# Kernel tuning notes

Hardware: AMD Instinct MI355X
Metric: run time of the kernel (lower is better)

Reference implementation:

```python
import jax, jax.numpy as jnp
import numpy as np


def _dequantize(packed, scales, zero_points):
    # packed: [out, in//2] holding two INT4 values per byte (low nibble = even col,
    # high nibble = odd col). Returns fp32 weight [out, in].
    low = (packed & 0xF).astype(jnp.float32)
    high = ((packed >> 4) & 0xF).astype(jnp.float32)
    w = jnp.stack([low, high], axis=-1).reshape(packed.shape[0], -1)  # [out, in]
    return (w - zero_points[:, None]) * scales[:, None]


def setup_inputs() -> dict:
    key = jax.random.key(0)
    k_x, k_w, k_s, k_z = jax.random.split(key, 4)
    TOKENS, IN_F, OUT_F = 8192, 4096, 14336
    x = jax.random.normal(k_x, (TOKENS, IN_F), dtype=jnp.float32)
    packed_weights = jax.random.randint(k_w, (OUT_F, IN_F // 2), 0, 256, dtype=jnp.int32)
    scales = jax.random.uniform(k_s, (OUT_F,), dtype=jnp.float32) * 0.01 + 1e-4
    zero_points = jax.random.uniform(k_z, (OUT_F,), dtype=jnp.float32) * 15.0
    return {"x": x, "packed_weights": packed_weights, "scales": scales,
            "zero_points": zero_points}


def reference(x, packed_weights, scales, zero_points):
    w_fp32 = _dequantize(packed_weights, scales, zero_points)  # [out, in]
    return x @ w_fp32.T  # [tokens, out]
```

## Files before the change

kernel.cpp:

```cpp
#include <hip/hip_runtime.h>
#include <hip/hip_bf16.h>


typedef __bf16 bf16x8 __attribute__((ext_vector_type(8)));
typedef __bf16 bf16x4 __attribute__((ext_vector_type(4)));
typedef float floatx4 __attribute__((ext_vector_type(4)));

#define M_DIM 8192
#define K_DIM 4096
#define N_DIM 14336
#define KB    (K_DIM / 2)

#define BM 128
#define BN 128
#define BK 64
#define LDSK 72

__global__ __launch_bounds__(256) void qgemm_bf16(
    const float* __restrict__ X,
    const int*   __restrict__ P,
    const float* __restrict__ S,
    const float* __restrict__ Z,
    float*       __restrict__ O)
{
    __shared__ __bf16 Alds[BM * LDSK];
    __shared__ __bf16 Blds[BN * LDSK];

    const int t  = threadIdx.x;
    const int bn = blockIdx.x;
    const int bm = blockIdx.y;

    const int rowA0 = t >> 4;
    const int c4    = t & 15;
    const int rowB0 = t >> 3;
    const int cB    = t & 7;

    const float* aG = X + (size_t)(bm * BM + rowA0) * K_DIM + c4 * 4;
    const int*   bG = P + (size_t)(bn * BN + rowB0) * KB    + cB * 4;

    float sreg[4], oreg[4];
    for (int it = 0; it < 4; ++it) {
        int r = bn * BN + rowB0 + 32 * it;
        float s = S[r], z = Z[r];
        sreg[it] = s;
        oreg[it] = -z * s;
    }

    const int lane = t & 63;
    const int wave = t >> 6;
    const int wm   = wave >> 1;
    const int wn   = wave & 1;
    const int fr   = lane & 15;
    const int quad = lane >> 4;

    floatx4 acc[4][4];
    for (int i = 0; i < 4; ++i)
        for (int j = 0; j < 4; ++j)
            acc[i][j] = (floatx4)0.0f;

    const __bf16* aBase = &Alds[(wm * 64 + fr) * LDSK + quad * 8];
    const __bf16* bBase = &Blds[(wn * 64 + fr) * LDSK + quad * 8];

    for (int kt = 0; kt < K_DIM / BK; ++kt) {
        float4 av[8];
        for (int it = 0; it < 8; ++it)
            av[it] = *(const float4*)(aG + (size_t)it * 16 * K_DIM);
        int4 bv[4];
        for (int it = 0; it < 4; ++it)
            bv[it] = *(const int4*)(bG + (size_t)it * 32 * KB);
        aG += BK;
        bG += BK / 2;

        for (int it = 0; it < 8; ++it) {
            bf16x4 w;
            w[0] = (__bf16)av[it].x;
            w[1] = (__bf16)av[it].y;
            w[2] = (__bf16)av[it].z;
            w[3] = (__bf16)av[it].w;
            *(bf16x4*)&Alds[(rowA0 + 16 * it) * LDSK + c4 * 4] = w;
        }
        for (int it = 0; it < 4; ++it) {
            const float s = sreg[it], o = oreg[it];
            const int b0 = bv[it].x, b1 = bv[it].y, b2 = bv[it].z, b3 = bv[it].w;
            bf16x8 w;
            w[0] = (__bf16)((float)(b0 & 15) * s + o);
            w[1] = (__bf16)((float)((b0 >> 4) & 15) * s + o);
            w[2] = (__bf16)((float)(b1 & 15) * s + o);
            w[3] = (__bf16)((float)((b1 >> 4) & 15) * s + o);
            w[4] = (__bf16)((float)(b2 & 15) * s + o);
            w[5] = (__bf16)((float)((b2 >> 4) & 15) * s + o);
            w[6] = (__bf16)((float)(b3 & 15) * s + o);
            w[7] = (__bf16)((float)((b3 >> 4) & 15) * s + o);
            *(bf16x8*)&Blds[(rowB0 + 32 * it) * LDSK + cB * 8] = w;
        }
        __syncthreads();

        for (int kk = 0; kk < BK; kk += 32) {
            bf16x8 af[4], bf[4];
            for (int i = 0; i < 4; ++i)
                af[i] = *(const bf16x8*)(aBase + (i * 16) * LDSK + kk);
            for (int j = 0; j < 4; ++j)
                bf[j] = *(const bf16x8*)(bBase + (j * 16) * LDSK + kk);
            for (int i = 0; i < 4; ++i)
                for (int j = 0; j < 4; ++j)
                    acc[i][j] = __builtin_amdgcn_mfma_f32_16x16x32_bf16(
                        af[i], bf[j], acc[i][j], 0, 0, 0);
        }
        __syncthreads();
    }

    for (int i = 0; i < 4; ++i) {
        const int row = bm * BM + wm * 64 + i * 16 + quad * 4;
        for (int j = 0; j < 4; ++j) {
            const int col = bn * BN + wn * 64 + j * 16 + fr;
            float* o = O + (size_t)row * N_DIM + col;
            for (int r = 0; r < 4; ++r)
                o[(size_t)r * N_DIM] = acc[i][j][r];
        }
    }
}

extern "C" void kernel_launch(void* const* d_in, const int* in_sizes, int n_in,
                              void* d_out, int out_size, void* d_ws, size_t ws_size,
                              hipStream_t stream) {
    const float* x = (const float*)d_in[0];
    const int*   p = (const int*)d_in[1];
    const float* s = (const float*)d_in[2];
    const float* z = (const float*)d_in[3];
    float* out = (float*)d_out;

    dim3 grid(N_DIM / BN, M_DIM / BM);
    qgemm_bf16<<<grid, 256, 0, stream>>>(x, p, s, z, out);
}
```

Before: 1.827 ms.

## Pre-convert X and dequantize W to bf16, then run async-LDS GEMM

Splits the fused kernel into three passes: convert X to bf16 and dequantize the INT4 weights to bf16 into workspace buffers, then run a plain bf16 GEMM. The GEMM loads tiles straight into LDS with global_load_lds and remaps workgroups with a swizzle so neighbouring blocks share L2 data. This removes the per-tile conversion and dequant work that every block repeated, and the register staging of loads. In exchange it writes and rereads about 180 MB of workspace, uses unpadded LDS rows that may cause bank conflicts, and falls back to the old kernel if the workspace is too small.

```diff
diff --git a/kernel.cpp b/kernel.cpp
--- a/kernel.cpp
+++ b/kernel.cpp
@@ -15,6 +15,126 @@
 #define BN 128
 #define BK 64
 #define LDSK 72
+
+__device__ __forceinline__ void async_ld16(const __bf16* g, __bf16* l) {
+    __builtin_amdgcn_global_load_lds(
+        (const __attribute__((address_space(1))) void*)g,
+        (__attribute__((address_space(3))) void*)l,
+        16, 0, 0);
+}
+
+__global__ __launch_bounds__(256) void cvt_x_kernel(
+    const float* __restrict__ X, __bf16* __restrict__ XB)
+{
+    const size_t n8 = (size_t)M_DIM * K_DIM / 8;
+    const size_t stride = (size_t)gridDim.x * blockDim.x;
+    for (size_t i = (size_t)blockIdx.x * blockDim.x + threadIdx.x; i < n8; i += stride) {
+        float4 a = ((const float4*)X)[2 * i];
+        float4 b = ((const float4*)X)[2 * i + 1];
+        bf16x8 w;
+        w[0] = (__bf16)a.x; w[1] = (__bf16)a.y; w[2] = (__bf16)a.z; w[3] = (__bf16)a.w;
+        w[4] = (__bf16)b.x; w[5] = (__bf16)b.y; w[6] = (__bf16)b.z; w[7] = (__bf16)b.w;
+        ((bf16x8*)XB)[i] = w;
+    }
+}
+
+__global__ __launch_bounds__(256) void dequant_w_kernel(
+    const int* __restrict__ P, const float* __restrict__ S,
+    const float* __restrict__ Z, __bf16* __restrict__ WB)
+{
+    const size_t n4 = (size_t)N_DIM * KB / 4;
+    const size_t stride = (size_t)gridDim.x * blockDim.x;
+    for (size_t i = (size_t)blockIdx.x * blockDim.x + threadIdx.x; i < n4; i += stride) {
+        const int row = (int)(i >> 9);
+        const float s = S[row];
+        const float o = -Z[row] * s;
+        int4 b = ((const int4*)P)[i];
+        bf16x8 w;
+        w[0] = (__bf16)((float)(b.x & 15) * s + o);
+        w[1] = (__bf16)((float)((b.x >> 4) & 15) * s + o);
+        w[2] = (__bf16)((float)(b.y & 15) * s + o);
+        w[3] = (__bf16)((float)((b.y >> 4) & 15) * s + o);
+        w[4] = (__bf16)((float)(b.z & 15) * s + o);
+        w[5] = (__bf16)((float)((b.z >> 4) & 15) * s + o);
+        w[6] = (__bf16)((float)(b.w & 15) * s + o);
+        w[7] = (__bf16)((float)((b.w >> 4) & 15) * s + o);
+        ((bf16x8*)WB)[i] = w;
+    }
+}
+
+__global__ __launch_bounds__(256) void gemm_bf16_2p(
+    const __bf16* __restrict__ A,
+    const __bf16* __restrict__ B,
+    float*        __restrict__ O)
+{
+    __shared__ __bf16 Alds[BM * BK];
+    __shared__ __bf16 Blds[BN * BK];
+
+    const int t    = threadIdx.x;
+    const int lane = t & 63;
+    const int wave = t >> 6;
+
+    const int nwg  = (N_DIM / BN) * (M_DIM / BM);
+    const int orig = blockIdx.x;
+    const int swz  = (orig & 7) * (nwg >> 3) + (orig >> 3);
+    const int bn   = swz % (N_DIM / BN);
+    const int bm   = swz / (N_DIM / BN);
+
+    const int srow = lane >> 3;
+    const int scol = (lane & 7) * 8;
+    const __bf16* aG = A + (size_t)(bm * BM + wave * 32 + srow) * K_DIM + scol;
+    const __bf16* bG = B + (size_t)(bn * BN + wave * 32 + srow) * K_DIM + scol;
+    __bf16* aL = &Alds[(wave * 32) * BK];
+    __bf16* bL = &Blds[(wave * 32) * BK];
+
+    const int wm   = wave >> 1;
+    const int wn   = wave & 1;
+    const int fr   = lane & 15;
+    const int quad = lane >> 4;
+
+    floatx4 acc[4][4];
+    for (int i = 0; i < 4; ++i)
+        for (int j = 0; j < 4; ++j)
+            acc[i][j] = (floatx4)0.0f;
+
+    const __bf16* aF = &Alds[(wm * 64 + fr) * BK + quad * 8];
+    const __bf16* bF = &Blds[(wn * 64 + fr) * BK + quad * 8];
+
+    for (int kt = 0; kt < K_DIM / BK; ++kt) {
+#pragma unroll
+        for (int i = 0; i < 4; ++i) {
+            async_ld16(aG + (size_t)(i * 8) * K_DIM, aL + i * 8 * BK);
+            async_ld16(bG + (size_t)(i * 8) * K_DIM, bL + i * 8 * BK);
+        }
+        aG += BK;
+        bG += BK;
+        __syncthreads();
+
+#pragma unroll
+        for (int kk = 0; kk < BK; kk += 32) {
+            bf16x8 af[4], bv[4];
+            for (int i = 0; i < 4; ++i)
+                af[i] = *(const bf16x8*)(aF + i * 16 * BK + kk);
+            for (int j = 0; j < 4; ++j)
+                bv[j] = *(const bf16x8*)(bF + j * 16 * BK + kk);
+            for (int i = 0; i < 4; ++i)
+                for (int j = 0; j < 4; ++j)
+                    acc[i][j] = __builtin_amdgcn_mfma_f32_16x16x32_bf16(
+                        af[i], bv[j], acc[i][j], 0, 0, 0);
+        }
+        __syncthreads();
+    }
+
+    for (int i = 0; i < 4; ++i) {
+        const int row = bm * BM + wm * 64 + i * 16 + quad * 4;
+        for (int j = 0; j < 4; ++j) {
+            const int col = bn * BN + wn * 64 + j * 16 + fr;
+            float* o = O + (size_t)row * N_DIM + col;
+            for (int r = 0; r < 4; ++r)
+                o[(size_t)r * N_DIM] = acc[i][j][r];
+        }
+    }
+}
 
 __global__ __launch_bounds__(256) void qgemm_bf16(
     const float* __restrict__ X,
@@ -129,6 +249,18 @@
     const float* z = (const float*)d_in[3];
     float* out = (float*)d_out;
 
-    dim3 grid(N_DIM / BN, M_DIM / BM);
-    qgemm_bf16<<<grid, 256, 0, stream>>>(x, p, s, z, out);
-}
+    const size_t bytesX = (size_t)M_DIM * K_DIM * 2;
+    const size_t bytesW = (size_t)N_DIM * K_DIM * 2;
+
+    if (d_ws != nullptr && ws_size >= bytesX + bytesW) {
+        __bf16* xb = (__bf16*)d_ws;
+        __bf16* wb = (__bf16*)((char*)d_ws + bytesX);
+        cvt_x_kernel<<<2048, 256, 0, stream>>>(x, xb);
+        dequant_w_kernel<<<2048, 256, 0, stream>>>(p, s, z, wb);
+        const int nwg = (N_DIM / BN) * (M_DIM / BM);
+        gemm_bf16_2p<<<nwg, 256, 0, stream>>>(xb, wb, out);
+    } else {
+        dim3 grid(N_DIM / BN, M_DIM / BM);
+        qgemm_bf16<<<grid, 256, 0, stream>>>(x, p, s, z, out);
+    }
+}
```

After: 1.873 ms. 2.5% more time.
